# Kernel optimization log

Hardware: AMD Instinct MI355X
Metric: run time of the kernel (lower is better)

## Reference

```python
import jax, jax.numpy as jnp
import numpy as np

EPS = 1e-5
K = 32          # nsample in PCT sample_and_group
S1, S2 = 512, 256


def _bn_relu(h, gamma, beta, axes):
    # BatchNorm1d in training mode: batch stats over (batch, length) per channel (last axis here)
    mu = jnp.mean(h, axes, keepdims=True)
    var = jnp.var(h, axes, keepdims=True)
    return jax.nn.relu((h - mu) * jax.lax.rsqrt(var + EPS) * gamma + beta)


def _index_points(points, idx):
    # points [B,N,C], idx [B,...] int -> [B,...,C]
    return jax.vmap(lambda p, i: p[i])(points, idx)


def _fps(xyz, npoint):
    # farthest point sampling; deterministic start at index 0. xyz [B,N,3] -> [B,npoint] int32
    B, N, _ = xyz.shape

    def body(carry, _):
        dmin, far = carry
        c = jnp.take_along_axis(xyz, far[:, None, None], axis=1)  # [B,1,3]
        dmin = jnp.minimum(dmin, jnp.sum((xyz - c) ** 2, -1))     # [B,N]
        return (dmin, jnp.argmax(dmin, -1).astype(jnp.int32)), far

    init = (jnp.full((B, N), 1e10, xyz.dtype), jnp.zeros((B,), jnp.int32))
    _, idxs = jax.lax.scan(body, init, None, length=npoint)
    return jnp.transpose(idxs)  # [B, npoint]


def _sg(features, xyz, s, w1, g1, b1, w2, g2, b2):
    # features [B,N,C], xyz [B,N,3] -> (new_xyz [B,s,3], out [B,s,out_ch])
    xyz_c = jax.lax.stop_gradient(xyz)
    fps_idx = _fps(xyz_c, s)                       # [B,s]
    new_xyz = _index_points(xyz, fps_idx)          # [B,s,3]
    new_pts = _index_points(features, fps_idx)     # [B,s,C]
    q = jax.lax.stop_gradient(new_xyz)
    # squared distances centers->all points, [B,s,N]
    d = (jnp.sum(q * q, -1)[:, :, None] + jnp.sum(xyz_c * xyz_c, -1)[:, None, :]
         - 2.0 * jnp.einsum('bsc,bnc->bsn', q, xyz_c))
    _, knn = jax.lax.top_k(-d, K)                  # [B,s,K] nearest neighbors
    grouped = _index_points(features, knn)         # [B,s,K,C]
    rel = grouped - new_pts[:, :, None, :]
    feat = jnp.concatenate([rel, jnp.broadcast_to(new_pts[:, :, None, :], rel.shape)], -1)  # [B,s,K,2C]
    h = _bn_relu(jnp.einsum('bskc,oc->bsko', feat, w1), g1, b1, (0, 1, 2))
    h = _bn_relu(jnp.einsum('bskc,oc->bsko', h, w2), g2, b2, (0, 1, 2))
    return new_xyz, jnp.max(h, axis=2)             # max over K neighbors -> [B,s,out]


def _forward(x, w1, g1, b1, w2, g2, b2,
             s1_w1, s1_g1, s1_b1, s1_w2, s1_g2, s1_b2,
             s2_w1, s2_g1, s2_b1, s2_w2, s2_g2, s2_b2):
    xyz = jnp.transpose(x, (0, 2, 1))                                # [B,N,3]
    f = _bn_relu(jnp.einsum('bcn,oc->bno', x, w1), g1, b1, (0, 1))   # [B,N,64]
    f = _bn_relu(jnp.einsum('bnc,oc->bno', f, w2), g2, b2, (0, 1))   # [B,N,64]
    xyz1, f1 = _sg(f, xyz, S1, s1_w1, s1_g1, s1_b1, s1_w2, s1_g2, s1_b2)   # [B,512,128]
    _, f2 = _sg(f1, xyz1, S2, s2_w1, s2_g1, s2_b1, s2_w2, s2_g2, s2_b2)    # [B,256,256]
    return jnp.transpose(f2, (0, 2, 1))                              # [B,256,256] channel-first


def setup_inputs() -> dict:
    key = jax.random.key(0)
    ks = jax.random.split(key, 8)
    B, N = 32, 4096
    inp = {"x": jax.random.normal(ks[0], (B, 3, N), jnp.float32)}

    def w(k, o, i):
        return jax.random.normal(k, (o, i), jnp.float32) * (1.0 / np.sqrt(i))

    inp["w1"] = w(ks[1], 64, 3);   inp["g1"] = jnp.ones((64,), jnp.float32);  inp["b1"] = jnp.zeros((64,), jnp.float32)
    inp["w2"] = w(ks[2], 64, 64);  inp["g2"] = jnp.ones((64,), jnp.float32);  inp["b2"] = jnp.zeros((64,), jnp.float32)
    inp["s1_w1"] = w(ks[3], 128, 128); inp["s1_g1"] = jnp.ones((128,), jnp.float32); inp["s1_b1"] = jnp.zeros((128,), jnp.float32)
    inp["s1_w2"] = w(ks[4], 128, 128); inp["s1_g2"] = jnp.ones((128,), jnp.float32); inp["s1_b2"] = jnp.zeros((128,), jnp.float32)
    inp["s2_w1"] = w(ks[5], 256, 256); inp["s2_g1"] = jnp.ones((256,), jnp.float32); inp["s2_b1"] = jnp.zeros((256,), jnp.float32)
    inp["s2_w2"] = w(ks[6], 256, 256); inp["s2_g2"] = jnp.ones((256,), jnp.float32); inp["s2_b2"] = jnp.zeros((256,), jnp.float32)
    return inp


def reference(x, w1, g1, b1, w2, g2, b2,
              s1_w1, s1_g1, s1_b1, s1_w2, s1_g2, s1_b2,
              s2_w1, s2_g1, s2_b1, s2_w2, s2_g2, s2_b2):
    return _forward(x, w1, g1, b1, w2, g2, b2,
                    s1_w1, s1_g1, s1_b1, s1_w2, s1_g2, s1_b2,
                    s2_w1, s2_g1, s2_b1, s2_w2, s2_g2, s2_b2)
```

## Files before the change

kernel.cpp:

```cpp
#include <hip/hip_runtime.h>

typedef short short8 __attribute__((ext_vector_type(8)));
typedef _Float16 h8 __attribute__((ext_vector_type(8)));
typedef float f32x4 __attribute__((ext_vector_type(4)));

#define DEVI __device__ __forceinline__

DEVI float h2f(short s) { return (float)__builtin_bit_cast(_Float16, s); }
DEVI short f2h(float f) { return __builtin_bit_cast(short, (_Float16)f); }
DEVI f32x4 mfma16(short8 a, short8 b, f32x4 c) {
  return __builtin_amdgcn_mfma_f32_16x16x32_f16(
      __builtin_bit_cast(h8, a), __builtin_bit_cast(h8, b), c, 0, 0, 0);
}

DEVI float wave_max_bcast(float v) {
  const int ID = 0xff800000;
  int x = __builtin_bit_cast(int, v);
#define STEPM(ctrl)                                                     \
  {                                                                     \
    int t = __builtin_amdgcn_update_dpp(ID, x, ctrl, 0xf, 0xf, false);  \
    x = __builtin_bit_cast(int, fmaxf(__builtin_bit_cast(float, x),     \
                                      __builtin_bit_cast(float, t)));   \
  }
  STEPM(0x111) STEPM(0x112) STEPM(0x114) STEPM(0x118) STEPM(0x142) STEPM(0x143)
#undef STEPM
  return __builtin_bit_cast(float, __builtin_amdgcn_readlane(x, 63));
}
DEVI float wave_min_bcast_f(float v) {
  const int ID = 0x7f800000;
  int x = __builtin_bit_cast(int, v);
#define STEPN(ctrl)                                                     \
  {                                                                     \
    int t = __builtin_amdgcn_update_dpp(ID, x, ctrl, 0xf, 0xf, false);  \
    x = __builtin_bit_cast(int, fminf(__builtin_bit_cast(float, x),     \
                                      __builtin_bit_cast(float, t)));   \
  }
  STEPN(0x111) STEPN(0x112) STEPN(0x114) STEPN(0x118) STEPN(0x142) STEPN(0x143)
#undef STEPN
  return __builtin_bit_cast(float, __builtin_amdgcn_readlane(x, 63));
}
DEVI unsigned wave_min_bcast_u(unsigned v) {
  const int ID = (int)0xffffffff;
  int x = (int)v;
#define STEPU(ctrl)                                                     \
  {                                                                     \
    int t = __builtin_amdgcn_update_dpp(ID, x, ctrl, 0xf, 0xf, false);  \
    x = (int)((unsigned)x < (unsigned)t ? (unsigned)x : (unsigned)t);   \
  }
  STEPU(0x111) STEPU(0x112) STEPU(0x114) STEPU(0x118) STEPU(0x142) STEPU(0x143)
#undef STEPU
  return (unsigned)__builtin_amdgcn_readlane(x, 63);
}
DEVI unsigned wave_iscan_add(unsigned v) {
  int x = (int)v, t;
  t = __builtin_amdgcn_update_dpp(0, x, 0x111, 0xf, 0xf, false); x += t;
  t = __builtin_amdgcn_update_dpp(0, x, 0x112, 0xf, 0xf, false); x += t;
  t = __builtin_amdgcn_update_dpp(0, x, 0x114, 0xf, 0xf, false); x += t;
  t = __builtin_amdgcn_update_dpp(0, x, 0x118, 0xf, 0xf, false); x += t;
  t = __builtin_amdgcn_update_dpp(0, x, 0x142, 0xa, 0xf, false); x += t;
  t = __builtin_amdgcn_update_dpp(0, x, 0x143, 0xc, 0xf, false); x += t;
  return (unsigned)x;
}

__global__ __launch_bounds__(256) void prep_kernel(
    const float* __restrict__ w2, const float* __restrict__ s1w2,
    const float* __restrict__ s2w2, const float* __restrict__ s1w1,
    const float* __restrict__ s2w1, short* __restrict__ w2b,
    short* __restrict__ s1w2b, short* __restrict__ s2w2b,
    short* __restrict__ W1pp, short* __restrict__ W2pp) {
  int i = blockIdx.x * 256 + threadIdx.x;
  if (i < 4096) {
    w2b[i] = f2h(w2[i]);
  } else if (i < 20480) {
    int j = i - 4096; s1w2b[j] = f2h(s1w2[j]);
  } else if (i < 86016) {
    int j = i - 20480; s2w2b[j] = f2h(s2w2[j]);
  } else if (i < 102400) {
    int j = i - 86016; int c = j & 127;
    float v = s1w1[j]; if (c >= 64) v -= s1w1[j - 64];
    W1pp[j] = f2h(v);
  } else if (i < 167936) {
    int j = i - 102400; int c = j & 255;
    float v = s2w1[j]; if (c >= 128) v -= s2w1[j - 128];
    W2pp[j] = f2h(v);
  }
}

__global__ __launch_bounds__(256) void stageA_kernel(
    const float* __restrict__ x, const float* __restrict__ w1,
    float* __restrict__ xyz, short* __restrict__ h0) {
  int i = blockIdx.x * 256 + threadIdx.x;
  int b = i >> 12, n = i & 4095;
  const float* xb = x + ((size_t)b * 3 << 12) + n;
  float x0 = xb[0], x1 = xb[4096], x2 = xb[8192];
  float* xp = xyz + (size_t)i * 3;
  xp[0] = x0; xp[1] = x1; xp[2] = x2;
  short* hp = h0 + ((size_t)i << 6);
#pragma unroll
  for (int o8 = 0; o8 < 8; ++o8) {
    short8 t;
#pragma unroll
    for (int j = 0; j < 8; ++j) {
      int o = o8 * 8 + j;
      float h = x0 * w1[o * 3] + x1 * w1[o * 3 + 1] + x2 * w1[o * 3 + 2];
      t[j] = f2h(h);
    }
    *reinterpret_cast<short8*>(hp + o8 * 8) = t;
  }
}


DEVI void stats64_body(int bid, int nb, int tid, const short* __restrict__ h,
                       float* __restrict__ partials, int M) {
  __shared__ float l0[256], l1[256];
  const int c = tid & 63, g = tid >> 6;
  float s0 = 0.f, s1 = 0.f;
  for (int m = bid * 4 + g; m < M; m += nb * 4) {
    float v = h2f(h[(size_t)m * 64 + c]);
    s0 += v; s1 += v * v;
  }
  l0[tid] = s0; l1[tid] = s1;
  __syncthreads();
  if (g == 0) {
    for (int w = 1; w < 4; ++w) { s0 += l0[c + w * 64]; s1 += l1[c + w * 64]; }
    partials[(size_t)c * nb + bid] = s0;
    partials[(size_t)(64 + c) * nb + bid] = s1;
  }
}

DEVI void reduce2_body(int c, int tid, const float* __restrict__ partials,
                       const float* __restrict__ gamma, const float* __restrict__ beta,
                       float* __restrict__ scale, float* __restrict__ shift,
                       int NB, int C, float invM) {
  __shared__ float l0[4], l1[4];
  const float* p0 = partials + (size_t)c * NB;
  const float* p1 = partials + (size_t)(C + c) * NB;
  float s0 = 0.f, s1 = 0.f;
  for (int i = tid; i < NB; i += 256) { s0 += p0[i]; s1 += p1[i]; }
#pragma unroll
  for (int off = 1; off < 64; off <<= 1) {
    s0 += __shfl_xor(s0, off);
    s1 += __shfl_xor(s1, off);
  }
  if ((tid & 63) == 0) { l0[tid >> 6] = s0; l1[tid >> 6] = s1; }
  __syncthreads();
  if (tid == 0) {
    s0 = l0[0] + l0[1] + l0[2] + l0[3];
    s1 = l1[0] + l1[1] + l1[2] + l1[3];
    float mean = s0 * invM;
    float var = fmaxf(s1 * invM - mean * mean, 0.f);
    float sc = gamma[c] / sqrtf(var + 1e-5f);
    scale[c] = sc;
    shift[c] = beta[c] - mean * sc;
  }
}

__global__ __launch_bounds__(256) void reduce2_kernel(
    const float* __restrict__ partials, const float* __restrict__ gamma,
    const float* __restrict__ beta, float* __restrict__ scale,
    float* __restrict__ shift, int NB, int C, float invM) {
  reduce2_body(blockIdx.x, threadIdx.x, partials, gamma, beta, scale, shift, NB, C, invM);
}

DEVI void apply_body(int bid, int tid, const short* __restrict__ h,
                     short* __restrict__ f, const float* __restrict__ scale,
                     const float* __restrict__ shift) {
  size_t i = ((size_t)bid * 256 + tid) * 8;
  int c0 = (int)(i & 63);
  short8 v = *reinterpret_cast<const short8*>(h + i);
  short8 o;
#pragma unroll
  for (int j = 0; j < 8; ++j) {
    float y = h2f(v[j]) * scale[c0 + j] + shift[c0 + j];
    o[j] = f2h(fmaxf(y, 0.f));
  }
  *reinterpret_cast<short8*>(f + i) = o;
}

template <int NPTS, int T>
DEVI void fps_seg_body(char* smemraw, int bid, int tid, const float* __restrict__ xyz,
                       int* __restrict__ out, float* __restrict__ xyzc, int nsel,
                       int it0, int it1, float* __restrict__ dming,
                       int* __restrict__ farg) {
  __builtin_amdgcn_s_setprio(1);
  constexpr int PT = NPTS / T;
  constexpr int NW = T / 64;
  float* sx = (float*)smemraw;
  float* sy = sx + NPTS;
  float* sz = sy + NPTS;
  float* wv = sz + NPTS;
  unsigned* wi = (unsigned*)(wv + 2 * NW);
  const int lane = tid & 63, wave = tid >> 6;
  const float* base = xyz + (size_t)bid * NPTS * 3;
  float px[PT], py[PT], pz[PT], dmin[PT];
#pragma unroll
  for (int j = 0; j < PT; ++j) {
    int n = j * T + tid;
    px[j] = base[n * 3]; py[j] = base[n * 3 + 1]; pz[j] = base[n * 3 + 2];
    sx[n] = px[j]; sy[n] = py[j]; sz[n] = pz[j];
  }
  int far;
  if (it0 == 0) {
#pragma unroll
    for (int j = 0; j < PT; ++j) dmin[j] = 1e10f;
    far = 0;
  } else {
#pragma unroll
    for (int j = 0; j < PT; ++j) dmin[j] = dming[(size_t)bid * NPTS + j * T + tid];
    far = farg[bid];
  }
  __syncthreads();
  float cx = sx[far], cy = sy[far], cz = sz[far];
  for (int it = it0; it < it1; ++it) {
    if (tid == 0) {
      out[bid * nsel + it] = far;
      if (xyzc) {
        float* xc = xyzc + ((size_t)bid * nsel + it) * 3;
        xc[0] = cx; xc[1] = cy; xc[2] = cz;
      }
    }
    float bv = -1.f;
#pragma unroll
    for (int j = 0; j < PT; ++j) {
      float dx = __fsub_rn(px[j], cx), dy = __fsub_rn(py[j], cy), dz = __fsub_rn(pz[j], cz);
      float d = __fadd_rn(__fadd_rn(__fmul_rn(dx, dx), __fmul_rn(dy, dy)), __fmul_rn(dz, dz));
      float dm = fminf(dmin[j], d);
      dmin[j] = dm;
      bv = fmaxf(bv, dm);
    }
    float wmv = wave_max_bcast(bv);
    unsigned ci = 0xffffffffu;
#pragma unroll
    for (int j = PT - 1; j >= 0; --j)
      if (dmin[j] == wmv) ci = (unsigned)(j * T + tid);
    unsigned wmi = wave_min_bcast_u(ci);
    const int bsel = it & 1;
    if (lane == 0) { wv[bsel * NW + wave] = wmv; wi[bsel * NW + wave] = wmi; }
    __syncthreads();
    const int e = lane & (NW - 1);
    float v = wv[bsel * NW + e];
    unsigned si = wi[bsel * NW + e];
#define CMB(ctrl)                                                                        \
  {                                                                                      \
    float v2 = __builtin_bit_cast(                                                       \
        float, __builtin_amdgcn_update_dpp(0, __builtin_bit_cast(int, v), ctrl, 0xf, 0xf, true)); \
    unsigned i2 = (unsigned)__builtin_amdgcn_update_dpp(0, (int)si, ctrl, 0xf, 0xf, true);\
    bool bt = (v2 > v) || (v2 == v && i2 < si);                                          \
    v = bt ? v2 : v; si = bt ? i2 : si;                                                  \
  }
    if constexpr (NW >= 2) CMB(0x121)
    if constexpr (NW >= 4) CMB(0x122)
    if constexpr (NW >= 8) CMB(0x124)
#undef CMB
    far = (int)si;
    cx = sx[far]; cy = sy[far]; cz = sz[far];
  }
  if (it1 < nsel) {
#pragma unroll
    for (int j = 0; j < PT; ++j) dming[(size_t)bid * NPTS + j * T + tid] = dmin[j];
    if (tid == 0) farg[bid] = far;
  }
}

template <int NPTS>
DEVI void fps2_wave_body(int bid, int lane, const float* __restrict__ xyz,
                         int* __restrict__ out, int nsel) {
  __builtin_amdgcn_s_setprio(1);
  constexpr int PT = NPTS / 64;
  const float* base = xyz + (size_t)bid * NPTS * 3;
  float px[PT], py[PT], pz[PT], dmin[PT];
#pragma unroll
  for (int j = 0; j < PT; ++j) {
    int n = j * 64 + lane;
    px[j] = base[n * 3]; py[j] = base[n * 3 + 1]; pz[j] = base[n * 3 + 2];
    dmin[j] = 1e10f;
  }
  int far = 0;
  float cx = __builtin_bit_cast(float, __builtin_amdgcn_readlane(__builtin_bit_cast(int, px[0]), 0));
  float cy = __builtin_bit_cast(float, __builtin_amdgcn_readlane(__builtin_bit_cast(int, py[0]), 0));
  float cz = __builtin_bit_cast(float, __builtin_amdgcn_readlane(__builtin_bit_cast(int, pz[0]), 0));
  for (int it = 0; it < nsel; ++it) {
    if (lane == 0) out[bid * nsel + it] = far;
    float bv = -1.f;
#pragma unroll
    for (int j = 0; j < PT; ++j) {
      float dx = __fsub_rn(px[j], cx), dy = __fsub_rn(py[j], cy), dz = __fsub_rn(pz[j], cz);
      float d = __fadd_rn(__fadd_rn(__fmul_rn(dx, dx), __fmul_rn(dy, dy)), __fmul_rn(dz, dz));
      float dm = fminf(dmin[j], d);
      dmin[j] = dm;
      bv = fmaxf(bv, dm);
    }
    float wmv = wave_max_bcast(bv);
    unsigned ci = 0xffffffffu;
#pragma unroll
    for (int j = PT - 1; j >= 0; --j)
      if (dmin[j] == wmv) ci = (unsigned)(j * 64 + lane);
    unsigned wmi = wave_min_bcast_u(ci);
    far = (int)wmi;
    const int jsel = (int)(wmi >> 6);
    float xc = px[0], yc = py[0], zc = pz[0];
#pragma unroll
    for (int j = 1; j < PT; ++j) {
      bool m = (jsel == j);
      xc = m ? px[j] : xc; yc = m ? py[j] : yc; zc = m ? pz[j] : zc;
    }
    const int lsel = (int)(wmi & 63u);
    cx = __builtin_bit_cast(float, __builtin_amdgcn_readlane(__builtin_bit_cast(int, xc), lsel));
    cy = __builtin_bit_cast(float, __builtin_amdgcn_readlane(__builtin_bit_cast(int, yc), lsel));
    cz = __builtin_bit_cast(float, __builtin_amdgcn_readlane(__builtin_bit_cast(int, zc), lsel));
  }
}

#define KNN_SMEM_BYTES ((4096 + 256 + 4 + 256 + 256) * 4)
template <int NPTS, int S>
DEVI void knn_body(char* smemraw, int bs, int tid, const float* __restrict__ pts,
                   const int* __restrict__ fpsidx, int* __restrict__ knn) {
  constexpr int PT = NPTS / 256;
  unsigned* hist = (unsigned*)smemraw;
  unsigned* csums = hist + 4096;
  unsigned* meta = csums + 256;
  float* bval = (float*)(meta + 4);
  unsigned* bidx = (unsigned*)(bval + 256);
  const int lane = tid & 63, wave = tid >> 6;
  const int b = bs / S;
  const int cidx = fpsidx[bs];
  const float* cp = pts + ((size_t)b * NPTS + cidx) * 3;
  const float qx = cp[0], qy = cp[1], qz = cp[2];
  const float qq = __fadd_rn(__fadd_rn(__fmul_rn(qx, qx), __fmul_rn(qy, qy)), __fmul_rn(qz, qz));
  const float* base = pts + (size_t)b * NPTS * 3;
  float d[PT]; unsigned u[PT];
#pragma unroll
  for (int j = 0; j < PT; ++j) {
    int n = j * 256 + tid;
    float x = base[n * 3], y = base[n * 3 + 1], z = base[n * 3 + 2];
    float pp = __fadd_rn(__fadd_rn(__fmul_rn(x, x), __fmul_rn(y, y)), __fmul_rn(z, z));
    float dot = __fadd_rn(__fadd_rn(__fmul_rn(qx, x), __fmul_rn(qy, y)), __fmul_rn(qz, z));
    d[j] = __fsub_rn(__fadd_rn(qq, pp), __fmul_rn(2.f, dot));
    unsigned bits = __builtin_bit_cast(unsigned, d[j]);
    unsigned m = (unsigned)((int)bits >> 31);
    u[j] = bits ^ (m | 0x80000000u);
  }
  {
    uint4 z4 = {0u, 0u, 0u, 0u};
    uint4* hq = (uint4*)hist;
    for (int i = tid; i < 1024; i += 256) hq[i] = z4;
    if (tid == 0) { meta[0] = 0; meta[3] = 0; }
  }
  __syncthreads();
#pragma unroll
  for (int j = 0; j < PT; ++j) atomicAdd(&hist[u[j] >> 20], 1u);
  __syncthreads();
  {
    const uint4* hq = (const uint4*)(hist + tid * 16);
    unsigned cs = 0;
#pragma unroll
    for (int q = 0; q < 4; ++q) {
      uint4 v = hq[q];
      cs += v.x + v.y + v.z + v.w;
    }
    csums[tid] = cs;
  }
  __syncthreads();
  if (wave == 0) {
    const int t4 = lane * 4;
    unsigned c0 = csums[t4], c1 = csums[t4 + 1], c2 = csums[t4 + 2], c3 = csums[t4 + 3];
    unsigned lt = c0 + c1 + c2 + c3;
    unsigned incl = wave_iscan_add(lt);
    unsigned excl = incl - lt;
    unsigned long long blt = __ballot(incl >= 32u);
    int L = __ffsll((long long)blt) - 1;
    if (lane == L) {
      unsigned cum = excl;
      int bucket = -1;
      unsigned cc[4] = {c0, c1, c2, c3};
#pragma unroll
      for (int q = 0; q < 4; ++q) {
        if (bucket < 0 && cum + cc[q] >= 32u) {
          int bbase = (t4 + q) * 16;
          for (int h = 0; h < 16; ++h) {
            unsigned hv = hist[bbase + h];
            if (cum + hv >= 32u) { bucket = bbase + h; break; }
            cum += hv;
          }
        } else if (bucket < 0) {
          cum += cc[q];
        }
      }
      meta[1] = (unsigned)bucket;
      meta[2] = cum;
    }
  }
  __syncthreads();
  const unsigned B = meta[1];
  const unsigned cb = meta[2];
  int* kout = knn + (size_t)bs * 32;
#pragma unroll
  for (int j = 0; j < PT; ++j) {
    unsigned bk = u[j] >> 20;
    if (bk < B) {
      unsigned p = atomicAdd(&meta[0], 1u);
      kout[p] = j * 256 + tid;
    } else if (bk == B) {
      unsigned p = atomicAdd(&meta[3], 1u);
      if (p < 256u) { bval[p] = d[j]; bidx[p] = (unsigned)(j * 256 + tid); }
    }
  }
  __syncthreads();
  const int m = 32 - (int)cb;
  if (wave == 0 && m > 0) {
    unsigned nb = meta[3]; if (nb > 256u) nb = 256u;
    float v0 = (lane < (int)nb) ? bval[lane] : 3.4e38f;
    unsigned i0 = (lane < (int)nb) ? bidx[lane] : 0xffffffffu;
    float v1 = (lane + 64 < (int)nb) ? bval[lane + 64] : 3.4e38f;
    unsigned i1 = (lane + 64 < (int)nb) ? bidx[lane + 64] : 0xffffffffu;
    float v2 = (lane + 128 < (int)nb) ? bval[lane + 128] : 3.4e38f;
    unsigned i2 = (lane + 128 < (int)nb) ? bidx[lane + 128] : 0xffffffffu;
    float v3 = (lane + 192 < (int)nb) ? bval[lane + 192] : 3.4e38f;
    unsigned i3 = (lane + 192 < (int)nb) ? bidx[lane + 192] : 0xffffffffu;
    for (int k = 0; k < m; ++k) {
      float lv = v0; unsigned li = i0;
      if (v1 < lv || (v1 == lv && i1 < li)) { lv = v1; li = i1; }
      if (v2 < lv || (v2 == lv && i2 < li)) { lv = v2; li = i2; }
      if (v3 < lv || (v3 == lv && i3 < li)) { lv = v3; li = i3; }
      float wmv = wave_min_bcast_f(lv);
      unsigned ci = (lv == wmv) ? li : 0xffffffffu;
      unsigned wmi = wave_min_bcast_u(ci);
      if (lane == 0) kout[cb + k] = (int)wmi;
      if (i0 == wmi) { v0 = 3.4e38f; i0 = 0xffffffffu; }
      if (i1 == wmi) { v1 = 3.4e38f; i1 = 0xffffffffu; }
      if (i2 == wmi) { v2 = 3.4e38f; i2 = 0xffffffffu; }
      if (i3 == wmi) { v3 = 3.4e38f; i3 = 0xffffffffu; }
    }
  }
}

template <int KD, int ND, bool GATHER, bool BNA, int NPTS, int S, int EPI>
DEVI void gemm_body(char* smemraw, int bid, int tid, int gemmBlocks,
                    const short* A, const int* KNNp, const int* FPSp,
                    const short* __restrict__ W, const float* __restrict__ bnscale,
                    const float* __restrict__ bnshift, short* Hout,
                    float* __restrict__ mmax, float* __restrict__ mmin,
                    float* __restrict__ partials) {
  constexpr int C = KD / 2;
  constexpr int NT = (ND > 128) ? 8 : ND / 16;
  constexpr int BR = (ND > 128) ? 64 : 128;
  constexpr int KC = (ND >= 256) ? 64 : KD;
  constexpr int LOG2KC = (KC == 64) ? 6 : 7;
  constexpr int NCH = KD / KC;
  constexpr int KTC = KC / 32;
  constexpr int LROW = KC + 8;
  constexpr int TROW = ND + 8;
  constexpr int LBB = ND * LROW * 2;
  constexpr int TBB = BR * TROW * 2;
  constexpr int LSOFF = (LBB > TBB) ? LBB : TBB;
  short* lb = (short*)smemraw;
  float* lstats = (float*)(smemraw + LSOFF);
  const int wave = tid >> 6, lane = tid & 63;
  const int rowOff = (ND > 128) ? (wave >> 1) * 32 : wave * 32;
  const int colOff = (ND > 128) ? (wave & 1) * 128 : 0;
  const int mBase = bid * BR + rowOff;
  for (int i = tid; i < 2 * ND; i += 256) lstats[i] = 0.f;

  const short* aptr[2][2];
#pragma unroll
  for (int rg = 0; rg < 2; ++rg) {
    int m = mBase + rg * 16 + (lane & 15);
    if constexpr (GATHER) {
      int idx = KNNp[m];
      int bb = m / (S * 32);
      int s = (m - bb * (S * 32)) >> 5;
      int fidx = FPSp[bb * S + s];
      aptr[rg][0] = A + ((size_t)bb * NPTS + idx) * C;
      aptr[rg][1] = A + ((size_t)bb * NPTS + fidx) * C;
    } else {
      aptr[rg][0] = A + (size_t)m * KD;
      aptr[rg][1] = A + (size_t)m * KD + C;
    }
  }
  const int koLane = (lane >> 4) * 8;
  f32x4 acc[2][NT];
#pragma unroll
  for (int rg = 0; rg < 2; ++rg)
#pragma unroll
    for (int nt = 0; nt < NT; ++nt) acc[rg][nt] = (f32x4){0.f, 0.f, 0.f, 0.f};

#pragma unroll
  for (int ch = 0; ch < NCH; ++ch) {
    __syncthreads();
    constexpr int SIT = (ND * KC) / 2048;
#pragma unroll
    for (int i = 0; i < SIT; ++i) {
      int e = i * 2048 + tid * 8;
      int n = e >> LOG2KC, kk = e & (KC - 1);
      short8 v = *reinterpret_cast<const short8*>(W + (size_t)n * KD + ch * KC + kk);
      *reinterpret_cast<short8*>(&lb[n * LROW + kk]) = v;
    }
    __syncthreads();
#pragma unroll
    for (int ktc = 0; ktc < KTC; ++ktc) {
      const int kt = ch * KTC + ktc;
      const int half = (kt * 32 >= C) ? 1 : 0;
      const int ko = kt * 32 + koLane;
      const int koh = ko - half * C;
      short8 afrag[2];
#pragma unroll
      for (int rg = 0; rg < 2; ++rg) {
        short8 a = *reinterpret_cast<const short8*>(aptr[rg][half] + koh);
        if constexpr (BNA) {
          const float* scp = bnscale + ko;
          const float* shp = bnshift + ko;
#pragma unroll
          for (int j = 0; j < 8; ++j) {
            float v = h2f(a[j]);
            v = fmaxf(v * scp[j] + shp[j], 0.f);
            a[j] = f2h(v);
          }
        }
        afrag[rg] = a;
      }
#pragma unroll
      for (int nt = 0; nt < NT; ++nt) {
        short8 bfr = *reinterpret_cast<const short8*>(
            &lb[(colOff + nt * 16 + (lane & 15)) * LROW + ktc * 32 + koLane]);
        acc[0][nt] = mfma16(afrag[0], bfr, acc[0][nt]);
        acc[1][nt] = mfma16(afrag[1], bfr, acc[1][nt]);
      }
    }
  }
  __syncthreads();

#pragma unroll
  for (int nt = 0; nt < NT; ++nt) {
    float s0 = 0.f, s1 = 0.f;
#pragma unroll
    for (int rg = 0; rg < 2; ++rg)
#pragma unroll
      for (int i = 0; i < 4; ++i) {
        float v = acc[rg][nt][i];
        s0 += v; s1 += v * v;
      }
    s0 += __shfl_xor(s0, 16); s0 += __shfl_xor(s0, 32);
    s1 += __shfl_xor(s1, 16); s1 += __shfl_xor(s1, 32);
    if (lane < 16) {
      atomicAdd(&lstats[colOff + nt * 16 + lane], s0);
      atomicAdd(&lstats[ND + colOff + nt * 16 + lane], s1);
    }
  }

  if constexpr (EPI == 0) {
#pragma unroll
    for (int rg = 0; rg < 2; ++rg)
#pragma unroll
      for (int nt = 0; nt < NT; ++nt)
#pragma unroll
        for (int i = 0; i < 4; ++i) {
          int r = rowOff + rg * 16 + (lane >> 4) * 4 + i;
          int n = colOff + nt * 16 + (lane & 15);
          lb[r * TROW + n] = f2h(acc[rg][nt][i]);
        }
    __syncthreads();
    constexpr int TPR = ND / 8;
    constexpr int RPI = 256 / TPR;
    const int r0 = tid / TPR, c0 = (tid % TPR) * 8;
#pragma unroll
    for (int it = 0; it < BR / RPI; ++it) {
      int r = it * RPI + r0;
      short8 v = *reinterpret_cast<const short8*>(&lb[r * TROW + c0]);
      *reinterpret_cast<short8*>(&Hout[(size_t)(bid * BR + r) * ND + c0]) = v;
    }
  } else {
    const int center = (bid * BR + rowOff) >> 5;
#pragma unroll
    for (int nt = 0; nt < NT; ++nt) {
      float mx = -3.4e38f, mn = 3.4e38f;
#pragma unroll
      for (int rg = 0; rg < 2; ++rg)
#pragma unroll
        for (int i = 0; i < 4; ++i) {
          float v = acc[rg][nt][i];
          mx = fmaxf(mx, v); mn = fminf(mn, v);
        }
      mx = fmaxf(mx, __shfl_xor(mx, 16)); mx = fmaxf(mx, __shfl_xor(mx, 32));
      mn = fminf(mn, __shfl_xor(mn, 16)); mn = fminf(mn, __shfl_xor(mn, 32));
      if (lane < 16) {
        mmax[(size_t)center * ND + colOff + nt * 16 + lane] = mx;
        mmin[(size_t)center * ND + colOff + nt * 16 + lane] = mn;
      }
    }
    __syncthreads();
  }
  for (int i = tid; i < 2 * ND; i += 256)
    partials[(size_t)i * gemmBlocks + bid] = lstats[i];
}


template <int FN, int FT>
__global__ __launch_bounds__(256, 1) void fps_stats_seg(
    int fpsBlocks, const float* fxyz, int* fout, float* fxyzc, int fnsel,
    int it0, int it1, float* dming, int* farg,
    const short* sh, float* sp, int sM, int snb) {
  extern __shared__ char smem[];
  if ((int)blockIdx.x < fpsBlocks)
    fps_seg_body<FN, FT>(smem, blockIdx.x, threadIdx.x, fxyz, fout, fxyzc, fnsel,
                         it0, it1, dming, farg);
  else
    stats64_body(blockIdx.x - fpsBlocks, snb, threadIdx.x, sh, sp, sM);
}

template <int FN, int FT, int KNPTS, int KS>
__global__ __launch_bounds__(256, 1) void fps_r2_knn_seg(
    int fpsBlocks, int compBlocks, const float* fxyz, int* fout, float* fxyzc,
    int fnsel, int it0, int it1, float* dming, int* farg,
    const float* partials, const float* gamma, const float* beta,
    float* scale, float* shift, int NB, int C, float invM,
    const float* kpts, const int* kfps, int* kout, int ks0) {
  extern __shared__ char smem[];
  const int bx = (int)blockIdx.x;
  if (bx < fpsBlocks) {
    fps_seg_body<FN, FT>(smem, bx, threadIdx.x, fxyz, fout, fxyzc, fnsel,
                         it0, it1, dming, farg);
  } else if (bx < fpsBlocks + compBlocks) {
    reduce2_body(bx - fpsBlocks, threadIdx.x, partials, gamma, beta, scale,
                 shift, NB, C, invM);
  } else {
    int kb = bx - fpsBlocks - compBlocks;
    int bs = (kb >> 7) * KS + ks0 + (kb & 127);
    knn_body<KNPTS, KS>(smem, bs, threadIdx.x, kpts, kfps, kout);
  }
}

template <int FN, int FT, int KD, int ND, bool BNA, int EPI, int KNPTS, int KS>
__global__ __launch_bounds__(256, 1) void fps_gemm_knn_seg(
    int fpsBlocks, int compBlocks, const float* fxyz, int* fout, float* fxyzc,
    int fnsel, int it0, int it1, float* dming, int* farg,
    const short* A, const short* W, const float* bnscale, const float* bnshift,
    short* Hout, float* partials,
    const float* kpts, const int* kfps, int* kout, int ks0) {
  extern __shared__ char smem[];
  const int bx = (int)blockIdx.x;
  if (bx < fpsBlocks) {
    fps_seg_body<FN, FT>(smem, bx, threadIdx.x, fxyz, fout, fxyzc, fnsel,
                         it0, it1, dming, farg);
  } else if (bx < fpsBlocks + compBlocks) {
    gemm_body<KD, ND, false, BNA, 1, 1, EPI>(smem, bx - fpsBlocks, threadIdx.x,
                                             compBlocks, A, nullptr, nullptr,
                                             W, bnscale, bnshift, Hout, nullptr,
                                             nullptr, partials);
  } else {
    int kb = bx - fpsBlocks - compBlocks;
    int bs = (kb >> 7) * KS + ks0 + (kb & 127);
    knn_body<KNPTS, KS>(smem, bs, threadIdx.x, kpts, kfps, kout);
  }
}

template <int NPTS, int S>
__global__ __launch_bounds__(256, 4) void apply_knn_kernel(
    int knnBlocks, const float* kpts, const int* kfps, int* kout, int ks0,
    const short* ah, short* af, const float* ascale, const float* ashift) {
  __shared__ __align__(16) char smem[KNN_SMEM_BYTES];
  const int bx = (int)blockIdx.x;
  if (bx < knnBlocks) {
    int bs = (bx >> 7) * S + ks0 + (bx & 127);
    knn_body<NPTS, S>(smem, bs, threadIdx.x, kpts, kfps, kout);
  } else {
    apply_body(bx - knnBlocks, threadIdx.x, ah, af, ascale, ashift);
  }
}

template <int KD, int ND, int NPTS, int S>
__global__ __launch_bounds__(256, 4) void mega1_kernel(
    int fpsBlocks, const float* f2xyz, int* f2out, int f2nsel,
    const short* A, const int* KNNp, const int* FPSp, const short* W,
    short* Hout, float* partials) {
  extern __shared__ char smem[];
  const int bx = (int)blockIdx.x;
  if (bx < fpsBlocks) {
    if (threadIdx.x < 64)
      fps2_wave_body<512>(bx, threadIdx.x, f2xyz, f2out, f2nsel);
  } else {
    int gb = bx - fpsBlocks;
    const int gB = (int)gridDim.x - fpsBlocks;
    const int q = gB >> 3;
    gb = (gb & 7) * q + (gb >> 3);
    gemm_body<KD, ND, true, false, NPTS, S, 0>(smem, gb, threadIdx.x, gB, A, KNNp,
                                               FPSp, W, nullptr, nullptr, Hout,
                                               nullptr, nullptr, partials);
  }
}

template <int KD, int ND, bool GATHER, bool BNA, int NPTS, int S, int EPI>
__global__ __launch_bounds__(256, 4) void gemm_kernel(
    const short* A, const int* KNNp, const int* FPSp, const short* W,
    const float* bnscale, const float* bnshift, short* Hout,
    float* mmax, float* mmin, float* partials) {
  extern __shared__ char smem[];
  int bid = (int)blockIdx.x;
  if constexpr (GATHER) {
    const int q = (int)gridDim.x >> 3;
    bid = (bid & 7) * q + (bid >> 3);
  }
  gemm_body<KD, ND, GATHER, BNA, NPTS, S, EPI>(smem, bid, threadIdx.x,
                                               gridDim.x, A, KNNp, FPSp, W, bnscale,
                                               bnshift, Hout, mmax, mmin, partials);
}

template <int NPTS, int S>
__global__ __launch_bounds__(256, 4) void maxpool_knn_kernel(
    int knnBlocks, const float* pts, const int* fpsidx, int* knn,
    const float* mmax, const float* mmin, const float* scale, const float* shift,
    short* f1) {
  __shared__ __align__(16) char smem[KNN_SMEM_BYTES];
  if ((int)blockIdx.x < knnBlocks) {
    knn_body<NPTS, S>(smem, blockIdx.x, threadIdx.x, pts, fpsidx, knn);
  } else {
    const int ctr = (blockIdx.x - knnBlocks) * 2 + (threadIdx.x >> 7);
    const int c = threadIdx.x & 127;
    const float sc = scale[c], sh = shift[c];
    float y = (sc >= 0.f) ? mmax[(size_t)ctr * 128 + c] : mmin[(size_t)ctr * 128 + c];
    f1[(size_t)ctr * 128 + c] = f2h(fmaxf(sc * y + sh, 0.f));
  }
}

__global__ __launch_bounds__(256) void maxpool_out_kernel(
    const float* __restrict__ mmax, const float* __restrict__ mmin,
    const float* __restrict__ scale, const float* __restrict__ shift,
    float* __restrict__ out) {
  const int bs = blockIdx.x, c = threadIdx.x;
  const int b = bs >> 8, s = bs & 255;
  const float sc = scale[c], sh = shift[c];
  float y = (sc >= 0.f) ? mmax[(size_t)bs * 256 + c] : mmin[(size_t)bs * 256 + c];
  out[((size_t)b << 16) + ((size_t)c << 8) + s] = fmaxf(sc * y + sh, 0.f);
}

extern "C" void kernel_launch(void* const* d_in, const int* in_sizes, int n_in,
                              void* d_out, int out_size, void* d_ws, size_t ws_size,
                              hipStream_t stream) {
  (void)in_sizes; (void)n_in; (void)out_size; (void)ws_size;
  const float* x    = (const float*)d_in[0];
  const float* w1   = (const float*)d_in[1];
  const float* g1   = (const float*)d_in[2];
  const float* b1   = (const float*)d_in[3];
  const float* w2   = (const float*)d_in[4];
  const float* g2   = (const float*)d_in[5];
  const float* b2   = (const float*)d_in[6];
  const float* s1w1 = (const float*)d_in[7];
  const float* s1g1 = (const float*)d_in[8];
  const float* s1b1 = (const float*)d_in[9];
  const float* s1w2 = (const float*)d_in[10];
  const float* s1g2 = (const float*)d_in[11];
  const float* s1b2 = (const float*)d_in[12];
  const float* s2w1 = (const float*)d_in[13];
  const float* s2g1 = (const float*)d_in[14];
  const float* s2b1 = (const float*)d_in[15];
  const float* s2w2 = (const float*)d_in[16];
  const float* s2g2 = (const float*)d_in[17];
  const float* s2b2 = (const float*)d_in[18];
  float* out = (float*)d_out;

  char* ws = (char*)d_ws;
  size_t off = 0;
  auto alloc = [&](size_t bytes) -> char* {
    size_t p = (off + 255) & ~(size_t)255;
    off = p + bytes;
    return ws + p;
  };

  float* xyz      = (float*)alloc(32ull * 4096 * 3 * 4);
  short* h0       = (short*)alloc(32ull * 4096 * 64 * 2);
  short* hb       = (short*)alloc(32ull * 4096 * 64 * 2);
  short* fb       = (short*)alloc(32ull * 4096 * 64 * 2);
  int*   fps1     = (int*)alloc(32ull * 512 * 4);
  float* xyzc1    = (float*)alloc(32ull * 512 * 3 * 4);
  int*   knn1     = (int*)alloc(32ull * 512 * 32 * 4);
  short* f1       = (short*)alloc(32ull * 512 * 128 * 2);
  int*   fps2     = (int*)alloc(32ull * 256 * 4);
  int*   knn2     = (int*)alloc(32ull * 256 * 32 * 4);
  float* dming    = (float*)alloc(32ull * 4096 * 4);
  int*   farg     = (int*)alloc(32 * 4);
  short* hbuf     = (short*)alloc(134217728ull);
  float* mm1max   = (float*)alloc(16384ull * 128 * 4);
  float* mm1min   = (float*)alloc(16384ull * 128 * 4);
  float* mm2max   = (float*)alloc(8192ull * 256 * 4);
  float* mm2min   = (float*)alloc(8192ull * 256 * 4);
  float* partials = (float*)alloc(2ull * 256 * 4096 * 4);
  float* scA  = (float*)alloc(64 * 4);  float* shA  = (float*)alloc(64 * 4);
  float* scBc = (float*)alloc(64 * 4);  float* shBc = (float*)alloc(64 * 4);
  float* sc1a = (float*)alloc(128 * 4); float* sh1a = (float*)alloc(128 * 4);
  float* sc1b = (float*)alloc(128 * 4); float* sh1b = (float*)alloc(128 * 4);
  float* sc2a = (float*)alloc(256 * 4); float* sh2a = (float*)alloc(256 * 4);
  float* sc2b = (float*)alloc(256 * 4); float* sh2b = (float*)alloc(256 * 4);
  short* w2b   = (short*)alloc(4096 * 2);
  short* s1w2b = (short*)alloc(16384 * 2);
  short* s2w2b = (short*)alloc(65536 * 2);
  short* W1pp  = (short*)alloc(16384 * 2);
  short* W2pp  = (short*)alloc(65536 * 2);

  prep_kernel<<<656, 256, 0, stream>>>(w2, s1w2, s2w2, s1w1, s2w1, w2b, s1w2b, s2w2b, W1pp, W2pp);
  stageA_kernel<<<512, 256, 0, stream>>>(x, w1, xyz, h0);

  fps_stats_seg<4096, 256><<<288, 256, 49216, stream>>>(
      32, xyz, fps1, xyzc1, 512, 0, 128, dming, farg, h0, partials, 131072, 256);
  fps_r2_knn_seg<4096, 256, 4096, 512><<<4192, 256, 49216, stream>>>(
      32, 64, xyz, fps1, xyzc1, 512, 128, 256, dming, farg,
      partials, g1, b1, scA, shA, 256, 64, 1.f / 131072.f,
      xyz, fps1, knn1, 0);
  fps_gemm_knn_seg<4096, 256, 64, 64, true, 0, 4096, 512><<<5152, 256, 49216, stream>>>(
      32, 1024, xyz, fps1, xyzc1, 512, 256, 384, dming, farg,
      h0, w2b, scA, shA, hb, partials,
      xyz, fps1, knn1, 128);
  fps_r2_knn_seg<4096, 256, 4096, 512><<<4192, 256, 49216, stream>>>(
      32, 64, xyz, fps1, xyzc1, 512, 384, 512, dming, farg,
      partials, g2, b2, scBc, shBc, 1024, 64, 1.f / 131072.f,
      xyz, fps1, knn1, 256);
  apply_knn_kernel<4096, 512><<<8192, 256, 0, stream>>>(
      4096, xyz, fps1, knn1, 384, hb, fb, scBc, shBc);

  mega1_kernel<128, 128, 4096, 512><<<4128, 256, 35840, stream>>>(
      32, xyzc1, fps2, 256, fb, knn1, fps1, W1pp, hbuf, partials);
  reduce2_kernel<<<128, 256, 0, stream>>>(partials, s1g1, s1b1, sc1a, sh1a, 4096, 128, 1.f / 524288.f);

  gemm_kernel<128, 128, false, true, 1, 1, 1><<<4096, 256, 35840, stream>>>(
      hbuf, nullptr, nullptr, s1w2b, sc1a, sh1a, nullptr, mm1max, mm1min, partials);
  reduce2_kernel<<<128, 256, 0, stream>>>(partials, s1g2, s1b2, sc1b, sh1b, 4096, 128, 1.f / 524288.f);

  maxpool_knn_kernel<512, 256><<<16384, 256, 0, stream>>>(
      8192, xyzc1, fps2, knn2, mm1max, mm1min, sc1b, sh1b, f1);

  gemm_kernel<256, 256, true, false, 512, 256, 0><<<4096, 256, 38912, stream>>>(
      f1, knn2, fps2, W2pp, nullptr, nullptr, hbuf, nullptr, nullptr, partials);
  reduce2_kernel<<<256, 256, 0, stream>>>(partials, s2g1, s2b1, sc2a, sh2a, 4096, 256, 1.f / 262144.f);
  gemm_kernel<256, 256, false, true, 1, 1, 1><<<4096, 256, 38912, stream>>>(
      hbuf, nullptr, nullptr, s2w2b, sc2a, sh2a, nullptr, mm2max, mm2min, partials);
  reduce2_kernel<<<256, 256, 0, stream>>>(partials, s2g2, s2b2, sc2b, sh2b, 4096, 256, 1.f / 262144.f);
  maxpool_out_kernel<<<8192, 256, 0, stream>>>(mm2max, mm2min, sc2b, sh2b, out);
}
```

Baseline: 838.4 us.

## Split second-stage FPS into segments overlapped across three kernels

The second farthest-point-sampling pass used to run as one single-wave block per batch inside the first GEMM kernel. It is now a 256-thread segmented FPS that carries its state (dmin and the current farthest index) through global buffers. Its iterations are split into three ranges, each piggybacked on the knn/apply kernel, the first GEMM kernel and the second GEMM kernel. This spreads the serial FPS latency so it hides behind the bulk work instead of forming the critical path of one kernel. The cost is extra global state writes and reads between segments, and the FPS blocks now use full blocks and shared memory alongside the other work.

Measured after the change: 795.2 us (median of 3 runs). 1.05x faster.

```diff
diff --git a/kernel.cpp b/kernel.cpp
--- a/kernel.cpp
+++ b/kernel.cpp
@@ -259,55 +259,6 @@
 #pragma unroll
     for (int j = 0; j < PT; ++j) dming[(size_t)bid * NPTS + j * T + tid] = dmin[j];
     if (tid == 0) farg[bid] = far;
-  }
-}
-
-template <int NPTS>
-DEVI void fps2_wave_body(int bid, int lane, const float* __restrict__ xyz,
-                         int* __restrict__ out, int nsel) {
-  __builtin_amdgcn_s_setprio(1);
-  constexpr int PT = NPTS / 64;
-  const float* base = xyz + (size_t)bid * NPTS * 3;
-  float px[PT], py[PT], pz[PT], dmin[PT];
-#pragma unroll
-  for (int j = 0; j < PT; ++j) {
-    int n = j * 64 + lane;
-    px[j] = base[n * 3]; py[j] = base[n * 3 + 1]; pz[j] = base[n * 3 + 2];
-    dmin[j] = 1e10f;
-  }
-  int far = 0;
-  float cx = __builtin_bit_cast(float, __builtin_amdgcn_readlane(__builtin_bit_cast(int, px[0]), 0));
-  float cy = __builtin_bit_cast(float, __builtin_amdgcn_readlane(__builtin_bit_cast(int, py[0]), 0));
-  float cz = __builtin_bit_cast(float, __builtin_amdgcn_readlane(__builtin_bit_cast(int, pz[0]), 0));
-  for (int it = 0; it < nsel; ++it) {
-    if (lane == 0) out[bid * nsel + it] = far;
-    float bv = -1.f;
-#pragma unroll
-    for (int j = 0; j < PT; ++j) {
-      float dx = __fsub_rn(px[j], cx), dy = __fsub_rn(py[j], cy), dz = __fsub_rn(pz[j], cz);
-      float d = __fadd_rn(__fadd_rn(__fmul_rn(dx, dx), __fmul_rn(dy, dy)), __fmul_rn(dz, dz));
-      float dm = fminf(dmin[j], d);
-      dmin[j] = dm;
-      bv = fmaxf(bv, dm);
-    }
-    float wmv = wave_max_bcast(bv);
-    unsigned ci = 0xffffffffu;
-#pragma unroll
-    for (int j = PT - 1; j >= 0; --j)
-      if (dmin[j] == wmv) ci = (unsigned)(j * 64 + lane);
-    unsigned wmi = wave_min_bcast_u(ci);
-    far = (int)wmi;
-    const int jsel = (int)(wmi >> 6);
-    float xc = px[0], yc = py[0], zc = pz[0];
-#pragma unroll
-    for (int j = 1; j < PT; ++j) {
-      bool m = (jsel == j);
-      xc = m ? px[j] : xc; yc = m ? py[j] : yc; zc = m ? pz[j] : zc;
-    }
-    const int lsel = (int)(wmi & 63u);
-    cx = __builtin_bit_cast(float, __builtin_amdgcn_readlane(__builtin_bit_cast(int, xc), lsel));
-    cy = __builtin_bit_cast(float, __builtin_amdgcn_readlane(__builtin_bit_cast(int, yc), lsel));
-    cz = __builtin_bit_cast(float, __builtin_amdgcn_readlane(__builtin_bit_cast(int, zc), lsel));
   }
 }
 
@@ -653,38 +604,64 @@
   }
 }
 
-template <int NPTS, int S>
-__global__ __launch_bounds__(256, 4) void apply_knn_kernel(
+template <int F2N, int NPTS, int S>
+__global__ __launch_bounds__(256, 4) void fps2_knn_apply_kernel(
+    int f2Blocks, const float* f2xyz, int* f2out, int f2nsel, int it0, int it1,
+    float* dming2, int* farg2,
     int knnBlocks, const float* kpts, const int* kfps, int* kout, int ks0,
     const short* ah, short* af, const float* ascale, const float* ashift) {
   __shared__ __align__(16) char smem[KNN_SMEM_BYTES];
   const int bx = (int)blockIdx.x;
-  if (bx < knnBlocks) {
-    int bs = (bx >> 7) * S + ks0 + (bx & 127);
+  if (bx < f2Blocks) {
+    fps_seg_body<F2N, 256>(smem, bx, threadIdx.x, f2xyz, f2out, nullptr, f2nsel,
+                           it0, it1, dming2, farg2);
+  } else if (bx < f2Blocks + knnBlocks) {
+    int kb = bx - f2Blocks;
+    int bs = (kb >> 7) * S + ks0 + (kb & 127);
     knn_body<NPTS, S>(smem, bs, threadIdx.x, kpts, kfps, kout);
   } else {
-    apply_body(bx - knnBlocks, threadIdx.x, ah, af, ascale, ashift);
-  }
-}
-
-template <int KD, int ND, int NPTS, int S>
+    apply_body(bx - f2Blocks - knnBlocks, threadIdx.x, ah, af, ascale, ashift);
+  }
+}
+
+template <int F2N, int KD, int ND, int NPTS, int S>
 __global__ __launch_bounds__(256, 4) void mega1_kernel(
-    int fpsBlocks, const float* f2xyz, int* f2out, int f2nsel,
+    int f2Blocks, const float* f2xyz, int* f2out, int f2nsel, int it0, int it1,
+    float* dming2, int* farg2,
     const short* A, const int* KNNp, const int* FPSp, const short* W,
     short* Hout, float* partials) {
   extern __shared__ char smem[];
   const int bx = (int)blockIdx.x;
-  if (bx < fpsBlocks) {
-    if (threadIdx.x < 64)
-      fps2_wave_body<512>(bx, threadIdx.x, f2xyz, f2out, f2nsel);
+  if (bx < f2Blocks) {
+    fps_seg_body<F2N, 256>(smem, bx, threadIdx.x, f2xyz, f2out, nullptr, f2nsel,
+                           it0, it1, dming2, farg2);
   } else {
-    int gb = bx - fpsBlocks;
-    const int gB = (int)gridDim.x - fpsBlocks;
+    int gb = bx - f2Blocks;
+    const int gB = (int)gridDim.x - f2Blocks;
     const int q = gB >> 3;
     gb = (gb & 7) * q + (gb >> 3);
     gemm_body<KD, ND, true, false, NPTS, S, 0>(smem, gb, threadIdx.x, gB, A, KNNp,
                                                FPSp, W, nullptr, nullptr, Hout,
                                                nullptr, nullptr, partials);
+  }
+}
+
+template <int F2N, int KD, int ND>
+__global__ __launch_bounds__(256, 4) void fps2_gemm_kernel(
+    int f2Blocks, const float* f2xyz, int* f2out, int f2nsel, int it0, int it1,
+    float* dming2, int* farg2,
+    const short* A, const short* W, const float* bnscale, const float* bnshift,
+    float* mmax, float* mmin, float* partials) {
+  extern __shared__ char smem[];
+  const int bx = (int)blockIdx.x;
+  if (bx < f2Blocks) {
+    fps_seg_body<F2N, 256>(smem, bx, threadIdx.x, f2xyz, f2out, nullptr, f2nsel,
+                           it0, it1, dming2, farg2);
+  } else {
+    gemm_body<KD, ND, false, true, 1, 1, 1>(smem, bx - f2Blocks, threadIdx.x,
+                                            (int)gridDim.x - f2Blocks, A, nullptr,
+                                            nullptr, W, bnscale, bnshift, nullptr,
+                                            mmax, mmin, partials);
   }
 }
 
@@ -777,6 +754,8 @@
   int*   knn2     = (int*)alloc(32ull * 256 * 32 * 4);
   float* dming    = (float*)alloc(32ull * 4096 * 4);
   int*   farg     = (int*)alloc(32 * 4);
+  float* dming2   = (float*)alloc(32ull * 512 * 4);
+  int*   farg2    = (int*)alloc(32 * 4);
   short* hbuf     = (short*)alloc(134217728ull);
   float* mm1max   = (float*)alloc(16384ull * 128 * 4);
   float* mm1min   = (float*)alloc(16384ull * 128 * 4);
@@ -812,15 +791,19 @@
       32, 64, xyz, fps1, xyzc1, 512, 384, 512, dming, farg,
       partials, g2, b2, scBc, shBc, 1024, 64, 1.f / 131072.f,
       xyz, fps1, knn1, 256);
-  apply_knn_kernel<4096, 512><<<8192, 256, 0, stream>>>(
+
+  fps2_knn_apply_kernel<512, 4096, 512><<<8224, 256, 0, stream>>>(
+      32, xyzc1, fps2, 256, 0, 86, dming2, farg2,
       4096, xyz, fps1, knn1, 384, hb, fb, scBc, shBc);
 
-  mega1_kernel<128, 128, 4096, 512><<<4128, 256, 35840, stream>>>(
-      32, xyzc1, fps2, 256, fb, knn1, fps1, W1pp, hbuf, partials);
+  mega1_kernel<512, 128, 128, 4096, 512><<<4128, 256, 35840, stream>>>(
+      32, xyzc1, fps2, 256, 86, 171, dming2, farg2,
+      fb, knn1, fps1, W1pp, hbuf, partials);
   reduce2_kernel<<<128, 256, 0, stream>>>(partials, s1g1, s1b1, sc1a, sh1a, 4096, 128, 1.f / 524288.f);
 
-  gemm_kernel<128, 128, false, true, 1, 1, 1><<<4096, 256, 35840, stream>>>(
-      hbuf, nullptr, nullptr, s1w2b, sc1a, sh1a, nullptr, mm1max, mm1min, partials);
+  fps2_gemm_kernel<512, 128, 128><<<4128, 256, 35840, stream>>>(
+      32, xyzc1, fps2, 256, 171, 256, dming2, farg2,
+      hbuf, s1w2b, sc1a, sh1a, mm1max, mm1min, partials);
   reduce2_kernel<<<128, 256, 0, stream>>>(partials, s1g2, s1b2, sc1b, sh1b, 4096, 128, 1.f / 524288.f);
 
   maxpool_knn_kernel<512, 256><<<16384, 256, 0, stream>>>(
```
